# Kernel tuning notes

Hardware: AMD Instinct MI355X
Metric: run time of the kernel (lower is better)

The kernel has to match this reference:

```python
import jax, jax.numpy as jnp
import numpy as np

EMBED_DIM = 128
B, N = 8, 2048


def entmax15(z):
    """Exact 1.5-entmax along the last axis (Peters & Martins 2019, sort-based)."""
    z = z / 2.0
    z = z - jnp.max(z, axis=-1, keepdims=True)  # shift-invariance -> numerical stability
    zs = -jnp.sort(-z, axis=-1)                 # descending sort
    n = z.shape[-1]
    k = jnp.arange(1, n + 1, dtype=z.dtype)
    mean = jnp.cumsum(zs, axis=-1) / k
    meansq = jnp.cumsum(zs * zs, axis=-1) / k
    ss = k * (meansq - mean * mean)
    delta = (1.0 - ss) / k
    delta_safe = jnp.where(delta > 0, delta, 1.0)
    tau = mean - jnp.where(delta > 0, jnp.sqrt(delta_safe), 0.0)
    support = jnp.sum((tau <= zs).astype(jnp.int32), axis=-1, keepdims=True)
    tau_star = jnp.take_along_axis(tau, support - 1, axis=-1)
    return jnp.square(jnp.maximum(z - tau_star, 0.0))


def setup_inputs() -> dict:
    key = jax.random.key(0)
    ks = jax.random.split(key, 6)
    s = 1.0 / np.sqrt(EMBED_DIM)  # torch nn.Linear default init range
    return {
        "x_c": jax.random.normal(ks[0], (B, N, EMBED_DIM), jnp.float32),
        "x_n": jax.random.normal(ks[1], (B, N, EMBED_DIM), jnp.float32),
        "Wq": jax.random.uniform(ks[2], (EMBED_DIM, EMBED_DIM), jnp.float32, -s, s),
        "bq": jax.random.uniform(ks[3], (EMBED_DIM,), jnp.float32, -s, s),
        "Wk": jax.random.uniform(ks[4], (EMBED_DIM, EMBED_DIM), jnp.float32, -s, s),
        "bk": jax.random.uniform(ks[5], (EMBED_DIM,), jnp.float32, -s, s),
    }


def reference(x_c, x_n, Wq, bq, Wk, bk):
    Q = x_c @ Wq.T + bq                      # [B,N,D]
    K = x_n @ Wk.T + bk                      # [B,N,D]
    A = jnp.einsum("bnd,bmd->bnm", Q, K) / jnp.sqrt(jnp.float32(EMBED_DIM))
    # entmax15 sparse normalization over keys; dropout is identity in eval mode
    return entmax15(A)
```

## Files before the change

### kernel.cpp

```cpp
#include <hip/hip_runtime.h>
#include <hip/hip_bf16.h>

#define BATCH 8
#define SEQ   2048
#define DIM   128
#define NROWS 16384
#define THETA_SPAN 22.62741699796952f

typedef __bf16    bf16x8   __attribute__((ext_vector_type(8)));
typedef float     floatx4  __attribute__((ext_vector_type(4)));
typedef _Float16  half2v   __attribute__((ext_vector_type(2)));

static __device__ __forceinline__ unsigned short f2bf(float v) {
    union { __hip_bfloat16 h; unsigned short u; } c;
    c.h = __float2bfloat16(v);
    return c.u;
}
static __device__ __forceinline__ float bf2f(unsigned short u) {
    union { unsigned int i; float f; } c;
    c.i = (unsigned int)u << 16;
    return c.f;
}
static __device__ __forceinline__ unsigned int f2h2(float a, float b) {
    union { _Float16 h; unsigned short u; } ca, cb;
    ca.h = (_Float16)a;
    cb.h = (_Float16)b;
    return (unsigned int)ca.u | ((unsigned int)cb.u << 16);
}

#if __has_builtin(__builtin_amdgcn_fdot2)
static __device__ __forceinline__ float fdot2acc(half2v a, half2v b, float c) {
    return __builtin_amdgcn_fdot2(a, b, c, false);
}
#else
static __device__ __forceinline__ float fdot2acc(half2v a, half2v b, float c) {
    return fmaf((float)a.y, (float)b.y, fmaf((float)a.x, (float)b.x, c));
}
#endif

__global__ void __launch_bounds__(256, 2)
proj_qk(const float* __restrict__ xq, const float* __restrict__ xn,
        const float* __restrict__ Wq, const float* __restrict__ bq,
        const float* __restrict__ Wk, const float* __restrict__ bk,
        unsigned short* __restrict__ Qb, unsigned short* __restrict__ Kb) {
    const int isK = blockIdx.y;
    const float* __restrict__ X    = isK ? xn : xq;
    const float* __restrict__ W    = isK ? Wk : Wq;
    const float* __restrict__ bias = isK ? bk : bq;

    __shared__ __align__(16) unsigned short SM[34816];
    unsigned short* XH = SM;
    unsigned short* XL = SM + 8704;
    unsigned short* WW = SM + 17408;

    const int tid  = threadIdx.x;
    const int lane = tid & 63;
    const int wv   = tid >> 6;
    const int l4   = lane & 15;
    const int quad = lane >> 4;
    const int row0 = blockIdx.x * 64;

#pragma unroll
    for (int i = 0; i < 8; ++i) {
        const int g  = tid + 256 * i;
        const int r  = g >> 5;
        const int c4 = g & 31;
        const float4 xv = *reinterpret_cast<const float4*>(
            X + (size_t)(row0 + r) * DIM + 4 * c4);
        union { ushort2 v[2]; unsigned short u[4]; } hh, ll;
        const float xf[4] = {xv.x, xv.y, xv.z, xv.w};
#pragma unroll
        for (int j = 0; j < 4; ++j) {
            const unsigned short h = f2bf(xf[j]);
            hh.u[j] = h;
            ll.u[j] = f2bf(xf[j] - bf2f(h));
        }
        *reinterpret_cast<uint2*>(&XH[r * 136 + 4 * c4]) =
            *reinterpret_cast<uint2*>(hh.u);
        *reinterpret_cast<uint2*>(&XL[r * 136 + 4 * c4]) =
            *reinterpret_cast<uint2*>(ll.u);
    }
#pragma unroll
    for (int i = 0; i < 16; ++i) {
        const int g  = tid + 256 * i;
        const int d  = g >> 5;
        const int c4 = g & 31;
        const float4 wvv = *reinterpret_cast<const float4*>(
            W + (size_t)d * DIM + 4 * c4);
        union { uint2 v; unsigned short u[4]; } pw;
        pw.u[0] = f2bf(wvv.x); pw.u[1] = f2bf(wvv.y);
        pw.u[2] = f2bf(wvv.z); pw.u[3] = f2bf(wvv.w);
        *reinterpret_cast<uint2*>(&WW[d * 136 + 4 * c4]) = pw.v;
    }
    __syncthreads();

    floatx4 acc[8];
    const floatx4 zerov = {};
#pragma unroll
    for (int mt = 0; mt < 8; ++mt) acc[mt] = zerov;

#pragma unroll
    for (int kt = 0; kt < 4; ++kt) {
        const int koff = kt * 32 + quad * 8;
        const bf16x8 xh = *reinterpret_cast<const bf16x8*>(
            &XH[(wv * 16 + l4) * 136 + koff]);
        const bf16x8 xl = *reinterpret_cast<const bf16x8*>(
            &XL[(wv * 16 + l4) * 136 + koff]);
#pragma unroll
        for (int mt = 0; mt < 8; ++mt) {
            const bf16x8 wf = *reinterpret_cast<const bf16x8*>(
                &WW[(mt * 16 + l4) * 136 + koff]);
            acc[mt] = __builtin_amdgcn_mfma_f32_16x16x32_bf16(wf, xh, acc[mt], 0, 0, 0);
            acc[mt] = __builtin_amdgcn_mfma_f32_16x16x32_bf16(wf, xl, acc[mt], 0, 0, 0);
        }
    }

    const int erow = wv * 16 + l4;
#pragma unroll
    for (int mt = 0; mt < 8; ++mt) {
        const float4 bv = *reinterpret_cast<const float4*>(bias + mt * 16 + quad * 4);
        const float bf[4] = {bv.x, bv.y, bv.z, bv.w};
        union { uint2 v; unsigned short u[4]; } hh;
#pragma unroll
        for (int r = 0; r < 4; ++r) hh.u[r] = f2bf(acc[mt][r] + bf[r]);
        *reinterpret_cast<uint2*>(&XH[erow * 136 + mt * 16 + quad * 4]) = hh.v;
    }
    __syncthreads();

    const int l    = tid & 15;
    const int kthi = tid >> 4;
    if (!isK) {
#pragma unroll
        for (int rr = 0; rr < 4; ++rr) {
            const int row = l + 16 * rr;
            const uint4 ph = *reinterpret_cast<const uint4*>(&XH[row * 136 + kthi * 8]);
            const size_t base = ((size_t)kthi * NROWS + row0 + row) * 8;
            *reinterpret_cast<uint4*>(Qb + base) = ph;
        }
    } else {
#pragma unroll
        for (int rr = 0; rr < 4; ++rr) {
            const int row = l + 16 * rr;
            const int grow = row0 + row;
            const int b    = grow >> 11;
            const int key  = grow & (SEQ - 1);
            const uint4 pk = *reinterpret_cast<const uint4*>(&XH[row * 136 + kthi * 8]);
            const size_t base = (((size_t)(b * 16) + kthi) * SEQ + key) * 8;
            *reinterpret_cast<uint4*>(Kb + base) = pk;
        }
    }
}

__global__ void __launch_bounds__(512, 4)
attn_fused(const __bf16* __restrict__ Qb, const __bf16* __restrict__ Kb,
           float* __restrict__ out) {
    __shared__ unsigned int SW[8 * 2056];
    const int tid  = threadIdx.x;
    const int wv   = tid >> 6;
    const int lane = tid & 63;
    const int l4   = lane & 15;
    const int quad = lane >> 4;
    const int row0 = blockIdx.x * 16;
    const int b    = row0 >> 11;
    const int key0 = wv * 256;

    {
        floatx4 acc[16];
        const floatx4 zerov = {};
#pragma unroll
        for (int t = 0; t < 16; ++t) acc[t] = zerov;

        const size_t qbase = ((size_t)quad * NROWS + row0 + l4) * 8;
        const size_t kbase = (((size_t)(b * 16) + quad) * SEQ + key0 + l4) * 8;
        const size_t qstep = (size_t)4 * NROWS * 8;
        const size_t kstep = (size_t)4 * SEQ * 8;

#pragma unroll
        for (int kt = 0; kt < 4; ++kt) {
            const bf16x8 ah = *reinterpret_cast<const bf16x8*>(Qb + qbase + kt * qstep);
            const __bf16* kc = Kb + kbase + kt * kstep;
#pragma unroll
            for (int t = 0; t < 16; ++t) {
                const bf16x8 bkv = *reinterpret_cast<const bf16x8*>(kc + (size_t)t * 128);
                acc[t] = __builtin_amdgcn_mfma_f32_16x16x32_bf16(ah, bkv, acc[t], 0, 0, 0);
            }
        }
#pragma unroll
        for (int t = 0; t < 16; ++t) {
            const int key = key0 + t * 16 + l4;
            SW[(2 * quad + 0) * 2056 + key] = f2h2(acc[t][0], acc[t][1]);
            SW[(2 * quad + 1) * 2056 + key] = f2h2(acc[t][2], acc[t][3]);
        }
    }
    __syncthreads();

    const int g  = wv >> 1;
    const int sp = wv & 1;

    const unsigned int* Sw = &SW[(2 * g + sp) * 2056];
    unsigned int raw[32];
#pragma unroll
    for (int c = 0; c < 32; ++c) raw[c] = Sw[c * 64 + lane];

    half2v z0[16], z1[16];
#pragma unroll
    for (int i = 0; i < 16; ++i) {
        union { unsigned int u; half2v h; } c0, c1;
        c0.u = __builtin_amdgcn_perm(raw[2 * i + 1], raw[2 * i], 0x05040100u);
        c1.u = __builtin_amdgcn_perm(raw[2 * i + 1], raw[2 * i], 0x07060302u);
        z0[i] = c0.h;
        z1[i] = c1.h;
    }

    const half2v hzero = {(_Float16)0.0f, (_Float16)0.0f};
    const half2v hone  = {(_Float16)1.0f, (_Float16)1.0f};

    float m0 = -1e30f, m1 = -1e30f;
#pragma unroll
    for (int i = 0; i < 16; ++i) {
        m0 = fmaxf(m0, fmaxf((float)z0[i].x, (float)z0[i].y));
        m1 = fmaxf(m1, fmaxf((float)z1[i].x, (float)z1[i].y));
    }
#pragma unroll
    for (int off = 32; off >= 1; off >>= 1) {
        m0 = fmaxf(m0, __shfl_xor(m0, off, 64));
        m1 = fmaxf(m1, __shfl_xor(m1, off, 64));
    }

    float th0 = m0 - THETA_SPAN;
    float th1 = m1 - THETA_SPAN;
    for (int it = 0; it < 7; ++it) {
        const _Float16 t0h = (_Float16)th0;
        const _Float16 t1h = (_Float16)th1;
        const half2v n0 = {(_Float16)-t0h, (_Float16)-t0h};
        const half2v n1 = {(_Float16)-t1h, (_Float16)-t1h};
        float f0 = 0.0f, f1 = 0.0f, g0 = 0.0f, g1 = 0.0f;
#pragma unroll
        for (int i = 0; i < 16; ++i) {
            half2v d0 = z0[i] + n0;
            half2v d1 = z1[i] + n1;
            d0 = __builtin_elementwise_max(d0, hzero);
            d1 = __builtin_elementwise_max(d1, hzero);
            f0 = fdot2acc(d0, d0, f0);
            f1 = fdot2acc(d1, d1, f1);
            g0 = fdot2acc(d0, hone, g0);
            g1 = fdot2acc(d1, hone, g1);
        }
#pragma unroll
        for (int off = 32; off >= 1; off >>= 1) {
            f0 += __shfl_xor(f0, off, 64);
            f1 += __shfl_xor(f1, off, 64);
            g0 += __shfl_xor(g0, off, 64);
            g1 += __shfl_xor(g1, off, 64);
        }
        th0 += (f0 - 512.0f) / (2.0f * g0);
        th1 += (f1 - 512.0f) / (2.0f * g1);
    }

    float* o0 = out + (size_t)(row0 + 4 * g + 2 * sp + 0) * SEQ + lane;
    float* o1 = out + (size_t)(row0 + 4 * g + 2 * sp + 1) * SEQ + lane;
#pragma unroll
    for (int i = 0; i < 16; ++i) {
        const float a0 = fmaxf((float)z0[i].x - th0, 0.0f);
        const float a1 = fmaxf((float)z0[i].y - th0, 0.0f);
        const float b0 = fmaxf((float)z1[i].x - th1, 0.0f);
        const float b1 = fmaxf((float)z1[i].y - th1, 0.0f);
        __builtin_nontemporal_store(a0 * a0 * (1.0f / 512.0f), o0 + (size_t)(2 * i) * 64);
        __builtin_nontemporal_store(a1 * a1 * (1.0f / 512.0f), o0 + (size_t)(2 * i + 1) * 64);
        __builtin_nontemporal_store(b0 * b0 * (1.0f / 512.0f), o1 + (size_t)(2 * i) * 64);
        __builtin_nontemporal_store(b1 * b1 * (1.0f / 512.0f), o1 + (size_t)(2 * i + 1) * 64);
    }
}

extern "C" void kernel_launch(void* const* d_in, const int* in_sizes, int n_in,
                              void* d_out, int out_size, void* d_ws, size_t ws_size,
                              hipStream_t stream) {
    const float* x_c = (const float*)d_in[0];
    const float* x_n = (const float*)d_in[1];
    const float* Wq  = (const float*)d_in[2];
    const float* bq  = (const float*)d_in[3];
    const float* Wk  = (const float*)d_in[4];
    const float* bk  = (const float*)d_in[5];
    float* out = (float*)d_out;

    char* ws = (char*)d_ws;
    unsigned short* Qbl = (unsigned short*)ws;
    unsigned short* Kbl = (unsigned short*)(ws + ((size_t)4 << 20));

    proj_qk<<<dim3(NROWS / 64, 2), 256, 0, stream>>>(
        x_c, x_n, Wq, bq, Wk, bk, Qbl, Kbl);
    attn_fused<<<NROWS / 16, 512, 0, stream>>>(
        (const __bf16*)Qbl, (const __bf16*)Kbl, out);
}
```

Measured before the change: 184.4 us.

## Process 32 query rows per block with 16 waves sharing K fragments

The fused attention kernel now handles 32 query rows per block with 1024 threads instead of 16 rows with 512. Each wave covers 128 keys for two 16-row groups, so every K fragment it loads feeds two MFMAs, which halves K global traffic per output. Shared memory doubles to about 131 KB per block and the block size grows, which likely cuts resident blocks per CU and may lower occupancy.

```diff
diff --git a/kernel.cpp b/kernel.cpp
--- a/kernel.cpp
+++ b/kernel.cpp
@@ -151,53 +151,58 @@
     }
 }
 
-__global__ void __launch_bounds__(512, 4)
+__global__ void __launch_bounds__(1024, 4)
 attn_fused(const __bf16* __restrict__ Qb, const __bf16* __restrict__ Kb,
            float* __restrict__ out) {
-    __shared__ unsigned int SW[8 * 2056];
+    __shared__ unsigned int SW[16 * 2056];
     const int tid  = threadIdx.x;
     const int wv   = tid >> 6;
     const int lane = tid & 63;
     const int l4   = lane & 15;
     const int quad = lane >> 4;
-    const int row0 = blockIdx.x * 16;
-    const int b    = row0 >> 11;
-    const int key0 = wv * 256;
+    const int b    = blockIdx.x >> 6;
+    const int rb   = blockIdx.x & 63;
+    const int row0 = (b << 11) + (rb << 5);
+    const int key0 = wv << 7;
 
     {
-        floatx4 acc[16];
+        floatx4 acc[2][8];
         const floatx4 zerov = {};
 #pragma unroll
-        for (int t = 0; t < 16; ++t) acc[t] = zerov;
-
-        const size_t qbase = ((size_t)quad * NROWS + row0 + l4) * 8;
-        const size_t kbase = (((size_t)(b * 16) + quad) * SEQ + key0 + l4) * 8;
-        const size_t qstep = (size_t)4 * NROWS * 8;
-        const size_t kstep = (size_t)4 * SEQ * 8;
+        for (int rg = 0; rg < 2; ++rg)
+#pragma unroll
+            for (int t = 0; t < 8; ++t) acc[rg][t] = zerov;
+
+        const size_t qbase0 = ((size_t)quad * NROWS + row0 + l4) * 8;
+        const size_t qbase1 = ((size_t)quad * NROWS + row0 + 16 + l4) * 8;
+        const size_t kbase  = (((size_t)(b * 16) + quad) * SEQ + key0 + l4) * 8;
+        const size_t qstep  = (size_t)4 * NROWS * 8;
+        const size_t kstep  = (size_t)4 * SEQ * 8;
 
 #pragma unroll
         for (int kt = 0; kt < 4; ++kt) {
-            const bf16x8 ah = *reinterpret_cast<const bf16x8*>(Qb + qbase + kt * qstep);
+            const bf16x8 ah0 = *reinterpret_cast<const bf16x8*>(Qb + qbase0 + kt * qstep);
+            const bf16x8 ah1 = *reinterpret_cast<const bf16x8*>(Qb + qbase1 + kt * qstep);
             const __bf16* kc = Kb + kbase + kt * kstep;
 #pragma unroll
-            for (int t = 0; t < 16; ++t) {
+            for (int t = 0; t < 8; ++t) {
                 const bf16x8 bkv = *reinterpret_cast<const bf16x8*>(kc + (size_t)t * 128);
-                acc[t] = __builtin_amdgcn_mfma_f32_16x16x32_bf16(ah, bkv, acc[t], 0, 0, 0);
+                acc[0][t] = __builtin_amdgcn_mfma_f32_16x16x32_bf16(ah0, bkv, acc[0][t], 0, 0, 0);
+                acc[1][t] = __builtin_amdgcn_mfma_f32_16x16x32_bf16(ah1, bkv, acc[1][t], 0, 0, 0);
             }
         }
 #pragma unroll
-        for (int t = 0; t < 16; ++t) {
-            const int key = key0 + t * 16 + l4;
-            SW[(2 * quad + 0) * 2056 + key] = f2h2(acc[t][0], acc[t][1]);
-            SW[(2 * quad + 1) * 2056 + key] = f2h2(acc[t][2], acc[t][3]);
-        }
+        for (int rg = 0; rg < 2; ++rg)
+#pragma unroll
+            for (int t = 0; t < 8; ++t) {
+                const int key = key0 + t * 16 + l4;
+                SW[(8 * rg + 2 * quad + 0) * 2056 + key] = f2h2(acc[rg][t][0], acc[rg][t][1]);
+                SW[(8 * rg + 2 * quad + 1) * 2056 + key] = f2h2(acc[rg][t][2], acc[rg][t][3]);
+            }
     }
     __syncthreads();
 
-    const int g  = wv >> 1;
-    const int sp = wv & 1;
-
-    const unsigned int* Sw = &SW[(2 * g + sp) * 2056];
+    const unsigned int* Sw = &SW[wv * 2056];
     unsigned int raw[32];
 #pragma unroll
     for (int c = 0; c < 32; ++c) raw[c] = Sw[c * 64 + lane];
@@ -257,8 +262,8 @@
         th1 += (f1 - 512.0f) / (2.0f * g1);
     }
 
-    float* o0 = out + (size_t)(row0 + 4 * g + 2 * sp + 0) * SEQ + lane;
-    float* o1 = out + (size_t)(row0 + 4 * g + 2 * sp + 1) * SEQ + lane;
+    float* o0 = out + (size_t)(row0 + 2 * wv + 0) * SEQ + lane;
+    float* o1 = out + (size_t)(row0 + 2 * wv + 1) * SEQ + lane;
 #pragma unroll
     for (int i = 0; i < 16; ++i) {
         const float a0 = fmaxf((float)z0[i].x - th0, 0.0f);
@@ -289,6 +294,6 @@
 
     proj_qk<<<dim3(NROWS / 64, 2), 256, 0, stream>>>(
         x_c, x_n, Wq, bq, Wk, bk, Qbl, Kbl);
-    attn_fused<<<NROWS / 16, 512, 0, stream>>>(
+    attn_fused<<<NROWS / 32, 1024, 0, stream>>>(
         (const __bf16*)Qbl, (const __bf16*)Kbl, out);
 }
```

After: 191.6 us. 3.9% more time.
